# Optimization experiments

Measured on AMD Instinct MI355X. Metric: run time of the kernel, lower is better.

The kernel has to match this reference:

```python
import jax, jax.numpy as jnp
import numpy as np

B, C, H, W, P = 16, 512, 64, 64, 32


def setup_inputs() -> dict:
    key = jax.random.key(0)
    k1, k2, k3 = jax.random.split(key, 3)
    inputs = jax.random.normal(k1, (B, C, H, W), dtype=jnp.float32)
    weight = jax.random.uniform(k2, (P, C, 1, 1), dtype=jnp.float32)
    smooth_factor = jax.random.normal(k3, (P,), dtype=jnp.float32)
    return {"inputs": inputs, "weight": weight, "smooth_factor": smooth_factor}


def reference(inputs, weight, smooth_factor):
    b, c, h, w = inputs.shape
    p = weight.shape[0]
    n = h * w
    centers = weight.reshape(p, c)                      # [P,C]
    x = inputs.reshape(b, c, n)                         # [B,C,N]

    # distance-based logits: 2<c,x> - |x|^2 - |c|^2, clamped at 0
    cx = jnp.einsum('pc,bcn->bpn', centers, x)          # [B,P,N]
    x_sq = jnp.sum(x * x, axis=1, keepdims=True)        # [B,1,N]
    c_sq = jnp.sum(centers * centers, axis=1)[None, :, None]  # [1,P,1]
    beta = jax.nn.sigmoid(smooth_factor)                # [P]
    logits = jnp.minimum(2.0 * cx - x_sq - c_sq, 0.0) / beta[None, :, None]
    assign = jax.nn.softmax(logits, axis=1)             # [B,P,N]

    # assignment-weighted pooling
    qx = jnp.einsum('bpn,bcn->bpc', assign, x)          # [B,P,C]
    sum_ass = jnp.clip(jnp.sum(assign, axis=2, keepdims=True), 1e-5)  # [B,P,1]
    sigma = jnp.sqrt(beta / 2.0)                        # [P]
    out = (qx / sum_ass - centers[None, :, :]) / sigma[None, :, None]

    # L2-normalize over channel dim (torch F.normalize, eps=1e-12)
    norm = jnp.sqrt(jnp.sum(out * out, axis=2, keepdims=True))
    outputs = out / jnp.maximum(norm, 1e-12)
    outputs_t = jnp.transpose(outputs, (0, 2, 1))       # [B,C,P]
    assign_map = assign.reshape(b, p, h, w)             # [B,P,H,W]
    return outputs_t, assign_map
```

## Files before the change

kernel.cpp:

```cpp
#include <hip/hip_runtime.h>

constexpr int BB = 16;
constexpr int CC = 512;
constexpr int PP = 32;
constexpr int NN = 4096;
constexpr int TN = 128;

using f32x4 = __attribute__((ext_vector_type(4))) float;
using bf16x8 = __attribute__((ext_vector_type(8))) short;
typedef unsigned int uint;

__device__ __forceinline__ ushort f2bf(float f) {
  unsigned u = __builtin_bit_cast(unsigned, f);
  u += 0x7FFFu + ((u >> 16) & 1u);
  return (ushort)(u >> 16);
}

__device__ __forceinline__ uint packbf(float f) {
  uint u = __builtin_bit_cast(uint, f);
  uint hi = (u + (0x7FFFu + ((u >> 16) & 1u))) >> 16;
  float hif = __builtin_bit_cast(float, hi << 16);
  float lof = f - hif;
  uint ul = __builtin_bit_cast(uint, lof);
  uint lo = (ul + (0x7FFFu + ((ul >> 16) & 1u))) >> 16;
  return (lo << 16) | hi;
}

struct BfPair { bf16x8 hi, lo; };

__device__ __forceinline__ BfPair unpack8(const uint* __restrict__ row, int co) {
  uint4 a = *(const uint4*)(row + co);
  uint4 b = *(const uint4*)(row + co + 4);
  union { bf16x8 v; uint d[4]; } H, L;
  H.d[0] = (a.x & 0xffffu) | (a.y << 16); L.d[0] = (a.x >> 16) | (a.y & 0xffff0000u);
  H.d[1] = (a.z & 0xffffu) | (a.w << 16); L.d[1] = (a.z >> 16) | (a.w & 0xffff0000u);
  H.d[2] = (b.x & 0xffffu) | (b.y << 16); L.d[2] = (b.x >> 16) | (b.y & 0xffff0000u);
  H.d[3] = (b.z & 0xffffu) | (b.w << 16); L.d[3] = (b.z >> 16) | (b.w & 0xffff0000u);
  return {H.v, L.v};
}

__global__ __launch_bounds__(64) void prep_kernel(
    const float* __restrict__ w, const float* __restrict__ sf,
    float* __restrict__ beta, float* __restrict__ rbeta,
    float* __restrict__ csq, float* __restrict__ sum_ass) {
  int p = blockIdx.x;
  int t = threadIdx.x;
  if (t < 16) sum_ass[p * 16 + t] = 0.f;
  float s = 0.f;
  for (int i = t; i < CC; i += 64) {
    float v = w[p * CC + i];
    s = fmaf(v, v, s);
  }
#pragma unroll
  for (int off = 32; off; off >>= 1) s += __shfl_down(s, off);
  if (t == 0) {
    csq[p] = s;
    float e = __expf(-sf[p]);
    rbeta[p] = 1.f + e;
    beta[p] = 1.f / (1.f + e);
  }
}

__global__ __launch_bounds__(256, 3) void assign_kernel(
    const float* __restrict__ x, const float* __restrict__ w,
    const float* __restrict__ rbeta, const float* __restrict__ csq,
    float* __restrict__ assign_out, float* __restrict__ sum_ass) {
  __shared__ uint xpk[128][68];
  __shared__ uint cpk[32][68];
  __shared__ float xsqw[4][4][32];
  __shared__ float xsqf[128];

  int tid = threadIdx.x;
  int wv = tid >> 6, lane = tid & 63;
  int l15 = lane & 15, lg = lane >> 4;
  int b = blockIdx.x >> 5;
  int n0 = (blockIdx.x & 31) * TN;

  int c_s = tid >> 2;
  int q = tid & 3;
  int p_s = tid >> 3;
  int cq8 = (tid & 7) << 3;

  const float* xb = x + (size_t)b * CC * NN + n0 + q * 32;
  const float* wb = w + (size_t)p_s * CC + cq8;

  f32x4 acc[2][2];
#pragma unroll
  for (int i = 0; i < 2; ++i)
#pragma unroll
    for (int j = 0; j < 2; ++j) acc[i][j] = {0.f, 0.f, 0.f, 0.f};
  float sq[32];
#pragma unroll
  for (int i = 0; i < 32; ++i) sq[i] = 0.f;

  float4 xr[8], wr0, wr1;
#pragma unroll
  for (int i = 0; i < 8; ++i)
    xr[i] = *(const float4*)&xb[(size_t)c_s * NN + i * 4];
  wr0 = *(const float4*)&wb[0];
  wr1 = *(const float4*)&wb[4];
#pragma unroll
  for (int i = 0; i < 8; ++i) {
    float4 v = xr[i];
    sq[4 * i + 0] = fmaf(v.x, v.x, sq[4 * i + 0]);
    sq[4 * i + 1] = fmaf(v.y, v.y, sq[4 * i + 1]);
    sq[4 * i + 2] = fmaf(v.z, v.z, sq[4 * i + 2]);
    sq[4 * i + 3] = fmaf(v.w, v.w, sq[4 * i + 3]);
    int nr = q * 32 + i * 4;
    xpk[nr + 0][c_s] = packbf(v.x);
    xpk[nr + 1][c_s] = packbf(v.y);
    xpk[nr + 2][c_s] = packbf(v.z);
    xpk[nr + 3][c_s] = packbf(v.w);
  }
  {
    uint4 u0 = {packbf(wr0.x), packbf(wr0.y), packbf(wr0.z), packbf(wr0.w)};
    uint4 u1 = {packbf(wr1.x), packbf(wr1.y), packbf(wr1.z), packbf(wr1.w)};
    *(uint4*)&cpk[p_s][cq8] = u0;
    *(uint4*)&cpk[p_s][cq8 + 4] = u1;
  }
  __syncthreads();

  for (int c0 = 0; c0 < CC; c0 += 64) {
    bool more = (c0 + 64 < CC);
    if (more) {
#pragma unroll
      for (int i = 0; i < 8; ++i)
        xr[i] = *(const float4*)&xb[(size_t)(c0 + 64 + c_s) * NN + i * 4];
      wr0 = *(const float4*)&wb[c0 + 64];
      wr1 = *(const float4*)&wb[c0 + 64 + 4];
    }
#pragma unroll
    for (int ks = 0; ks < 2; ++ks) {
      int co = ks * 32 + lg * 8;
      BfPair A0 = unpack8(&cpk[l15][0], co);
      BfPair A1 = unpack8(&cpk[l15 + 16][0], co);
      BfPair B0 = unpack8(&xpk[wv * 32 + l15][0], co);
      BfPair B1 = unpack8(&xpk[wv * 32 + 16 + l15][0], co);
      acc[0][0] = __builtin_amdgcn_mfma_f32_16x16x32_bf16(A0.hi, B0.hi, acc[0][0], 0, 0, 0);
      acc[0][1] = __builtin_amdgcn_mfma_f32_16x16x32_bf16(A0.hi, B1.hi, acc[0][1], 0, 0, 0);
      acc[1][0] = __builtin_amdgcn_mfma_f32_16x16x32_bf16(A1.hi, B0.hi, acc[1][0], 0, 0, 0);
      acc[1][1] = __builtin_amdgcn_mfma_f32_16x16x32_bf16(A1.hi, B1.hi, acc[1][1], 0, 0, 0);
      acc[0][0] = __builtin_amdgcn_mfma_f32_16x16x32_bf16(A0.hi, B0.lo, acc[0][0], 0, 0, 0);
      acc[0][1] = __builtin_amdgcn_mfma_f32_16x16x32_bf16(A0.hi, B1.lo, acc[0][1], 0, 0, 0);
      acc[1][0] = __builtin_amdgcn_mfma_f32_16x16x32_bf16(A1.hi, B0.lo, acc[1][0], 0, 0, 0);
      acc[1][1] = __builtin_amdgcn_mfma_f32_16x16x32_bf16(A1.hi, B1.lo, acc[1][1], 0, 0, 0);
      acc[0][0] = __builtin_amdgcn_mfma_f32_16x16x32_bf16(A0.lo, B0.hi, acc[0][0], 0, 0, 0);
      acc[0][1] = __builtin_amdgcn_mfma_f32_16x16x32_bf16(A0.lo, B1.hi, acc[0][1], 0, 0, 0);
      acc[1][0] = __builtin_amdgcn_mfma_f32_16x16x32_bf16(A1.lo, B0.hi, acc[1][0], 0, 0, 0);
      acc[1][1] = __builtin_amdgcn_mfma_f32_16x16x32_bf16(A1.lo, B1.hi, acc[1][1], 0, 0, 0);
    }
    if (more) {
      __syncthreads();
#pragma unroll
      for (int i = 0; i < 8; ++i) {
        float4 v = xr[i];
        sq[4 * i + 0] = fmaf(v.x, v.x, sq[4 * i + 0]);
        sq[4 * i + 1] = fmaf(v.y, v.y, sq[4 * i + 1]);
        sq[4 * i + 2] = fmaf(v.z, v.z, sq[4 * i + 2]);
        sq[4 * i + 3] = fmaf(v.w, v.w, sq[4 * i + 3]);
        int nr = q * 32 + i * 4;
        xpk[nr + 0][c_s] = packbf(v.x);
        xpk[nr + 1][c_s] = packbf(v.y);
        xpk[nr + 2][c_s] = packbf(v.z);
        xpk[nr + 3][c_s] = packbf(v.w);
      }
      uint4 u0 = {packbf(wr0.x), packbf(wr0.y), packbf(wr0.z), packbf(wr0.w)};
      uint4 u1 = {packbf(wr1.x), packbf(wr1.y), packbf(wr1.z), packbf(wr1.w)};
      *(uint4*)&cpk[p_s][cq8] = u0;
      *(uint4*)&cpk[p_s][cq8 + 4] = u1;
      __syncthreads();
    }
  }

#pragma unroll
  for (int i = 0; i < 32; ++i) {
    sq[i] += __shfl_xor(sq[i], 4);
    sq[i] += __shfl_xor(sq[i], 8);
    sq[i] += __shfl_xor(sq[i], 16);
    sq[i] += __shfl_xor(sq[i], 32);
  }
  if ((lane >> 2) == 0) {
#pragma unroll
    for (int i = 0; i < 32; ++i) xsqw[wv][lane & 3][i] = sq[i];
  }
  __syncthreads();
  if (tid < 128)
    xsqf[tid] = xsqw[0][tid >> 5][tid & 31] + xsqw[1][tid >> 5][tid & 31] +
                xsqw[2][tid >> 5][tid & 31] + xsqw[3][tid >> 5][tid & 31];
  __syncthreads();

  float xsqn0 = xsqf[wv * 32 + l15];
  float xsqn1 = xsqf[wv * 32 + 16 + l15];

  float csqv[2][4], rbv[2][4];
#pragma unroll
  for (int pf = 0; pf < 2; ++pf)
#pragma unroll
    for (int i = 0; i < 4; ++i) {
      int p = pf * 16 + lg * 4 + i;
      csqv[pf][i] = csq[p];
      rbv[pf][i] = rbeta[p];
    }

  float L[2][2][4];
  float m0 = -3.4e38f, m1 = -3.4e38f;
#pragma unroll
  for (int pf = 0; pf < 2; ++pf)
#pragma unroll
    for (int i = 0; i < 4; ++i) {
      float l0 = fminf(2.f * acc[pf][0][i] - xsqn0 - csqv[pf][i], 0.f) * rbv[pf][i];
      float l1 = fminf(2.f * acc[pf][1][i] - xsqn1 - csqv[pf][i], 0.f) * rbv[pf][i];
      L[pf][0][i] = l0; L[pf][1][i] = l1;
      m0 = fmaxf(m0, l0); m1 = fmaxf(m1, l1);
    }
  m0 = fmaxf(m0, __shfl_xor(m0, 16)); m0 = fmaxf(m0, __shfl_xor(m0, 32));
  m1 = fmaxf(m1, __shfl_xor(m1, 16)); m1 = fmaxf(m1, __shfl_xor(m1, 32));
  float s0 = 0.f, s1 = 0.f;
#pragma unroll
  for (int pf = 0; pf < 2; ++pf)
#pragma unroll
    for (int i = 0; i < 4; ++i) {
      float e0 = __expf(L[pf][0][i] - m0);
      float e1 = __expf(L[pf][1][i] - m1);
      L[pf][0][i] = e0; L[pf][1][i] = e1;
      s0 += e0; s1 += e1;
    }
  s0 += __shfl_xor(s0, 16); s0 += __shfl_xor(s0, 32);
  s1 += __shfl_xor(s1, 16); s1 += __shfl_xor(s1, 32);
  float inv0 = 1.f / s0, inv1 = 1.f / s1;

  float* aoB = assign_out + (size_t)b * PP * NN + n0 + wv * 32 + l15;
  float sa[2][4];
#pragma unroll
  for (int pf = 0; pf < 2; ++pf)
#pragma unroll
    for (int i = 0; i < 4; ++i) {
      int p = pf * 16 + lg * 4 + i;
      float a0 = L[pf][0][i] * inv0;
      float a1 = L[pf][1][i] * inv1;
      aoB[(size_t)p * NN] = a0;
      aoB[(size_t)p * NN + 16] = a1;
      sa[pf][i] = a0 + a1;
    }
#pragma unroll
  for (int pf = 0; pf < 2; ++pf)
#pragma unroll
    for (int i = 0; i < 4; ++i) {
      float v = sa[pf][i];
      v += __shfl_xor(v, 1); v += __shfl_xor(v, 2);
      v += __shfl_xor(v, 4); v += __shfl_xor(v, 8);
      if (l15 == 0) atomicAdd(&sum_ass[b * PP + pf * 16 + lg * 4 + i], v);
    }
}

__global__ __launch_bounds__(256) void qx_kernel(
    const float* __restrict__ x, const float* __restrict__ assign,
    float* __restrict__ qx_part) {
  __shared__ ushort xbf[128][136];
  __shared__ ushort abf[32][136];

  int tid = threadIdx.x;
  int b = blockIdx.y;
  int kc = blockIdx.x >> 2;
  int ct = blockIdx.x & 3;
  int wv = tid >> 6, lane = tid & 63;
  int l15 = lane & 15, lg = lane >> 4;

  const float* xb = x + ((size_t)b * CC + ct * 128) * NN + kc * 512;
  const float* ab = assign + (size_t)b * PP * NN + kc * 512;

  int c_s = tid >> 1;
  int nh  = (tid & 1) << 6;
  int p_s = tid >> 3;
  int na  = (tid & 7) << 4;

  f32x4 acc[2][2];
#pragma unroll
  for (int i = 0; i < 2; ++i)
#pragma unroll
    for (int j = 0; j < 2; ++j) acc[i][j] = {0.f, 0.f, 0.f, 0.f};

  for (int ch = 0; ch < 4; ++ch) {
    int nb = ch * 128;
    if (ch) __syncthreads();
#pragma unroll
    for (int h = 0; h < 2; ++h) {
      float4 v[8];
#pragma unroll
      for (int i = 0; i < 8; ++i)
        v[i] = *(const float4*)&xb[(size_t)c_s * NN + nb + nh + h * 32 + i * 4];
#pragma unroll
      for (int i = 0; i < 8; ++i) {
        ushort4 u;
        u.x = f2bf(v[i].x); u.y = f2bf(v[i].y);
        u.z = f2bf(v[i].z); u.w = f2bf(v[i].w);
        *(ushort4*)&xbf[c_s][nh + h * 32 + i * 4] = u;
      }
    }
    {
      float4 v[4];
#pragma unroll
      for (int i = 0; i < 4; ++i)
        v[i] = *(const float4*)&ab[(size_t)p_s * NN + nb + na + i * 4];
#pragma unroll
      for (int i = 0; i < 4; ++i) {
        ushort4 u;
        u.x = f2bf(v[i].x); u.y = f2bf(v[i].y);
        u.z = f2bf(v[i].z); u.w = f2bf(v[i].w);
        *(ushort4*)&abf[p_s][na + i * 4] = u;
      }
    }
    __syncthreads();
#pragma unroll
    for (int ks = 0; ks < 4; ++ks) {
      int nf = ks * 32 + lg * 8;
      bf16x8 a0 = *(const bf16x8*)&abf[l15][nf];
      bf16x8 a1 = *(const bf16x8*)&abf[16 + l15][nf];
      bf16x8 b0 = *(const bf16x8*)&xbf[wv * 32 + l15][nf];
      bf16x8 b1 = *(const bf16x8*)&xbf[wv * 32 + 16 + l15][nf];
      acc[0][0] = __builtin_amdgcn_mfma_f32_16x16x32_bf16(a0, b0, acc[0][0], 0, 0, 0);
      acc[0][1] = __builtin_amdgcn_mfma_f32_16x16x32_bf16(a0, b1, acc[0][1], 0, 0, 0);
      acc[1][0] = __builtin_amdgcn_mfma_f32_16x16x32_bf16(a1, b0, acc[1][0], 0, 0, 0);
      acc[1][1] = __builtin_amdgcn_mfma_f32_16x16x32_bf16(a1, b1, acc[1][1], 0, 0, 0);
    }
  }

#pragma unroll
  for (int pf = 0; pf < 2; ++pf)
#pragma unroll
    for (int cf = 0; cf < 2; ++cf)
#pragma unroll
      for (int i = 0; i < 4; ++i) {
        int p = pf * 16 + lg * 4 + i;
        int c = ct * 128 + wv * 32 + cf * 16 + l15;
        qx_part[(((size_t)kc * BB + b) * PP + p) * CC + c] = acc[pf][cf][i];
      }
}

__global__ __launch_bounds__(256) void finalize_kernel(
    const float* __restrict__ qx_part, const float* __restrict__ w,
    const float* __restrict__ beta, const float* __restrict__ sum_ass,
    float* __restrict__ out_t) {
  int b = blockIdx.x >> 5;
  int p = blockIdx.x & 31;
  int tid = threadIdx.x;
  int wave = tid >> 6, lane = tid & 63;

  float inv_sa = 1.f / fmaxf(sum_ass[b * PP + p], 1e-5f);
  float rsig = rsqrtf(0.5f * beta[p]);

  int c0 = tid, c1 = tid + 256;
  float q0 = 0.f, q1 = 0.f;
#pragma unroll
  for (int kc = 0; kc < 8; ++kc) {
    const float* row = qx_part + (((size_t)kc * BB + b) * PP + p) * CC;
    q0 += row[c0];
    q1 += row[c1];
  }
  const float* wrow = w + (size_t)p * CC;
  float t0 = (q0 * inv_sa - wrow[c0]) * rsig;
  float t1 = (q1 * inv_sa - wrow[c1]) * rsig;

  float nr = t0 * t0 + t1 * t1;
#pragma unroll
  for (int off = 32; off; off >>= 1) nr += __shfl_down(nr, off);
  __shared__ float red[4];
  if (lane == 0) red[wave] = nr;
  __syncthreads();
  float norm2 = red[0] + red[1] + red[2] + red[3];
  float scale = 1.f / fmaxf(sqrtf(norm2), 1e-12f);

  float* ob = out_t + (size_t)b * CC * PP + p;
  ob[(size_t)c0 * PP] = t0 * scale;
  ob[(size_t)c1 * PP] = t1 * scale;
}

extern "C" void kernel_launch(void* const* d_in, const int* in_sizes, int n_in,
                              void* d_out, int out_size, void* d_ws,
                              size_t ws_size, hipStream_t stream) {
  const float* x = (const float*)d_in[0];
  const float* w = (const float*)d_in[1];
  const float* sf = (const float*)d_in[2];

  float* out_t = (float*)d_out;
  float* assign = out_t + (size_t)BB * CC * PP;

  float* ws = (float*)d_ws;
  float* beta = ws;
  float* rbeta = ws + 32;
  float* csq = ws + 64;
  float* sum_ass = ws + 96;
  float* qx_part = ws + 608;

  prep_kernel<<<PP, 64, 0, stream>>>(w, sf, beta, rbeta, csq, sum_ass);
  assign_kernel<<<BB * 32, 256, 0, stream>>>(x, w, rbeta, csq, assign,
                                             sum_ass);
  qx_kernel<<<dim3(32, BB), 256, 0, stream>>>(x, assign, qx_part);
  finalize_kernel<<<BB * PP, 256, 0, stream>>>(qx_part, w, beta, sum_ass,
                                               out_t);
}
```

Baseline: 88.89 us.

## Fuse assignment-weighted pooling into assign kernel with atomic qx accumulation

The qx GEMM moves into the assign kernel. Softmax outputs go straight to shared memory as bf16, and the block re-reads its own x tile in 128-channel chunks to run the MFMA pooling. Partial qx results are accumulated with global atomicAdd into a memset-zeroed buffer, which removes the separate qx kernel, its re-read of the assignment map, and the partial-sum reduction in finalize. In exchange there are many float atomics (512 blocks each adding 32x512 values), a second pass over x that may hit in cache, and a summation order that is no longer deterministic.

Result: slower. 95.37 us (+7.3%).

```diff
diff --git a/kernel.cpp b/kernel.cpp
--- a/kernel.cpp
+++ b/kernel.cpp
@@ -42,10 +42,9 @@
 __global__ __launch_bounds__(64) void prep_kernel(
     const float* __restrict__ w, const float* __restrict__ sf,
     float* __restrict__ beta, float* __restrict__ rbeta,
-    float* __restrict__ csq, float* __restrict__ sum_ass) {
+    float* __restrict__ csq) {
   int p = blockIdx.x;
   int t = threadIdx.x;
-  if (t < 16) sum_ass[p * 16 + t] = 0.f;
   float s = 0.f;
   for (int i = t; i < CC; i += 64) {
     float v = w[p * CC + i];
@@ -61,14 +60,17 @@
   }
 }
 
-__global__ __launch_bounds__(256, 3) void assign_kernel(
+__global__ __launch_bounds__(256, 3) void fused_kernel(
     const float* __restrict__ x, const float* __restrict__ w,
-    const float* __restrict__ rbeta, const float* __restrict__ csq,
-    float* __restrict__ assign_out, float* __restrict__ sum_ass) {
+    const float* __restrict__ rbeta_, const float* __restrict__ csq_,
+    float* __restrict__ assign_out, float* __restrict__ sum_ass,
+    float* __restrict__ qx) {
   __shared__ uint xpk[128][68];
   __shared__ uint cpk[32][68];
   __shared__ float xsqw[4][4][32];
   __shared__ float xsqf[128];
+  ushort(*xt)[136] = (ushort(*)[136]) & xpk[0][0];
+  ushort(*abf)[136] = (ushort(*)[136]) & cpk[0][0];
 
   int tid = threadIdx.x;
   int wv = tid >> 6, lane = tid & 63;
@@ -198,8 +200,8 @@
 #pragma unroll
     for (int i = 0; i < 4; ++i) {
       int p = pf * 16 + lg * 4 + i;
-      csqv[pf][i] = csq[p];
-      rbv[pf][i] = rbeta[p];
+      csqv[pf][i] = csq_[p];
+      rbv[pf][i] = rbeta_[p];
     }
 
   float L[2][2][4];
@@ -230,7 +232,6 @@
   float inv0 = 1.f / s0, inv1 = 1.f / s1;
 
   float* aoB = assign_out + (size_t)b * PP * NN + n0 + wv * 32 + l15;
-  float sa[2][4];
 #pragma unroll
   for (int pf = 0; pf < 2; ++pf)
 #pragma unroll
@@ -240,105 +241,68 @@
       float a1 = L[pf][1][i] * inv1;
       aoB[(size_t)p * NN] = a0;
       aoB[(size_t)p * NN + 16] = a1;
-      sa[pf][i] = a0 + a1;
-    }
-#pragma unroll
-  for (int pf = 0; pf < 2; ++pf)
-#pragma unroll
-    for (int i = 0; i < 4; ++i) {
-      float v = sa[pf][i];
+      abf[p][wv * 32 + l15] = f2bf(a0);
+      abf[p][wv * 32 + 16 + l15] = f2bf(a1);
+      float v = a0 + a1;
       v += __shfl_xor(v, 1); v += __shfl_xor(v, 2);
       v += __shfl_xor(v, 4); v += __shfl_xor(v, 8);
-      if (l15 == 0) atomicAdd(&sum_ass[b * PP + pf * 16 + lg * 4 + i], v);
-    }
-}
-
-__global__ __launch_bounds__(256) void qx_kernel(
-    const float* __restrict__ x, const float* __restrict__ assign,
-    float* __restrict__ qx_part) {
-  __shared__ ushort xbf[128][136];
-  __shared__ ushort abf[32][136];
-
-  int tid = threadIdx.x;
-  int b = blockIdx.y;
-  int kc = blockIdx.x >> 2;
-  int ct = blockIdx.x & 3;
-  int wv = tid >> 6, lane = tid & 63;
-  int l15 = lane & 15, lg = lane >> 4;
-
-  const float* xb = x + ((size_t)b * CC + ct * 128) * NN + kc * 512;
-  const float* ab = assign + (size_t)b * PP * NN + kc * 512;
-
-  int c_s = tid >> 1;
-  int nh  = (tid & 1) << 6;
-  int p_s = tid >> 3;
-  int na  = (tid & 7) << 4;
-
-  f32x4 acc[2][2];
-#pragma unroll
-  for (int i = 0; i < 2; ++i)
-#pragma unroll
-    for (int j = 0; j < 2; ++j) acc[i][j] = {0.f, 0.f, 0.f, 0.f};
+      if (l15 == 0) atomicAdd(&sum_ass[b * PP + p], v);
+    }
+
+  int c_s2 = tid >> 1;
+  int nh2 = (tid & 1) << 6;
+  const float* xg = x + (size_t)b * CC * NN + n0;
 
   for (int ch = 0; ch < 4; ++ch) {
-    int nb = ch * 128;
-    if (ch) __syncthreads();
+    __syncthreads();
 #pragma unroll
     for (int h = 0; h < 2; ++h) {
       float4 v[8];
 #pragma unroll
       for (int i = 0; i < 8; ++i)
-        v[i] = *(const float4*)&xb[(size_t)c_s * NN + nb + nh + h * 32 + i * 4];
+        v[i] = *(const float4*)&xg[(size_t)(ch * 128 + c_s2) * NN + nh2 + h * 32 + i * 4];
 #pragma unroll
       for (int i = 0; i < 8; ++i) {
         ushort4 u;
         u.x = f2bf(v[i].x); u.y = f2bf(v[i].y);
         u.z = f2bf(v[i].z); u.w = f2bf(v[i].w);
-        *(ushort4*)&xbf[c_s][nh + h * 32 + i * 4] = u;
+        *(ushort4*)&xt[c_s2][nh2 + h * 32 + i * 4] = u;
       }
     }
-    {
-      float4 v[4];
-#pragma unroll
-      for (int i = 0; i < 4; ++i)
-        v[i] = *(const float4*)&ab[(size_t)p_s * NN + nb + na + i * 4];
-#pragma unroll
-      for (int i = 0; i < 4; ++i) {
-        ushort4 u;
-        u.x = f2bf(v[i].x); u.y = f2bf(v[i].y);
-        u.z = f2bf(v[i].z); u.w = f2bf(v[i].w);
-        *(ushort4*)&abf[p_s][na + i * 4] = u;
+    __syncthreads();
+
+    f32x4 q2[2][2];
+#pragma unroll
+    for (int pf = 0; pf < 2; ++pf)
+#pragma unroll
+      for (int cf = 0; cf < 2; ++cf) q2[pf][cf] = {0.f, 0.f, 0.f, 0.f};
+#pragma unroll
+    for (int ks = 0; ks < 4; ++ks) {
+      int ko = ks * 32 + lg * 8;
+      bf16x8 A0 = *(const bf16x8*)&abf[l15][ko];
+      bf16x8 A1 = *(const bf16x8*)&abf[l15 + 16][ko];
+#pragma unroll
+      for (int cf = 0; cf < 2; ++cf) {
+        bf16x8 Bv = *(const bf16x8*)&xt[wv * 32 + cf * 16 + l15][ko];
+        q2[0][cf] = __builtin_amdgcn_mfma_f32_16x16x32_bf16(A0, Bv, q2[0][cf], 0, 0, 0);
+        q2[1][cf] = __builtin_amdgcn_mfma_f32_16x16x32_bf16(A1, Bv, q2[1][cf], 0, 0, 0);
       }
     }
-    __syncthreads();
-#pragma unroll
-    for (int ks = 0; ks < 4; ++ks) {
-      int nf = ks * 32 + lg * 8;
-      bf16x8 a0 = *(const bf16x8*)&abf[l15][nf];
-      bf16x8 a1 = *(const bf16x8*)&abf[16 + l15][nf];
-      bf16x8 b0 = *(const bf16x8*)&xbf[wv * 32 + l15][nf];
-      bf16x8 b1 = *(const bf16x8*)&xbf[wv * 32 + 16 + l15][nf];
-      acc[0][0] = __builtin_amdgcn_mfma_f32_16x16x32_bf16(a0, b0, acc[0][0], 0, 0, 0);
-      acc[0][1] = __builtin_amdgcn_mfma_f32_16x16x32_bf16(a0, b1, acc[0][1], 0, 0, 0);
-      acc[1][0] = __builtin_amdgcn_mfma_f32_16x16x32_bf16(a1, b0, acc[1][0], 0, 0, 0);
-      acc[1][1] = __builtin_amdgcn_mfma_f32_16x16x32_bf16(a1, b1, acc[1][1], 0, 0, 0);
-    }
-  }
-
-#pragma unroll
-  for (int pf = 0; pf < 2; ++pf)
-#pragma unroll
-    for (int cf = 0; cf < 2; ++cf)
-#pragma unroll
-      for (int i = 0; i < 4; ++i) {
-        int p = pf * 16 + lg * 4 + i;
-        int c = ct * 128 + wv * 32 + cf * 16 + l15;
-        qx_part[(((size_t)kc * BB + b) * PP + p) * CC + c] = acc[pf][cf][i];
-      }
+#pragma unroll
+    for (int pf = 0; pf < 2; ++pf)
+#pragma unroll
+      for (int cf = 0; cf < 2; ++cf)
+#pragma unroll
+        for (int i = 0; i < 4; ++i) {
+          int p = pf * 16 + lg * 4 + i;
+          int c = ch * 128 + wv * 32 + cf * 16 + l15;
+          atomicAdd(&qx[((size_t)b * PP + p) * CC + c], q2[pf][cf][i]);
+        }
+  }
 }
 
 __global__ __launch_bounds__(256) void finalize_kernel(
-    const float* __restrict__ qx_part, const float* __restrict__ w,
+    const float* __restrict__ qx, const float* __restrict__ w,
     const float* __restrict__ beta, const float* __restrict__ sum_ass,
     float* __restrict__ out_t) {
   int b = blockIdx.x >> 5;
@@ -350,16 +314,10 @@
   float rsig = rsqrtf(0.5f * beta[p]);
 
   int c0 = tid, c1 = tid + 256;
-  float q0 = 0.f, q1 = 0.f;
-#pragma unroll
-  for (int kc = 0; kc < 8; ++kc) {
-    const float* row = qx_part + (((size_t)kc * BB + b) * PP + p) * CC;
-    q0 += row[c0];
-    q1 += row[c1];
-  }
+  const float* qrow = qx + ((size_t)b * PP + p) * CC;
   const float* wrow = w + (size_t)p * CC;
-  float t0 = (q0 * inv_sa - wrow[c0]) * rsig;
-  float t1 = (q1 * inv_sa - wrow[c1]) * rsig;
+  float t0 = (qrow[c0] * inv_sa - wrow[c0]) * rsig;
+  float t1 = (qrow[c1] * inv_sa - wrow[c1]) * rsig;
 
   float nr = t0 * t0 + t1 * t1;
 #pragma unroll
@@ -390,12 +348,12 @@
   float* rbeta = ws + 32;
   float* csq = ws + 64;
   float* sum_ass = ws + 96;
-  float* qx_part = ws + 608;
-
-  prep_kernel<<<PP, 64, 0, stream>>>(w, sf, beta, rbeta, csq, sum_ass);
-  assign_kernel<<<BB * 32, 256, 0, stream>>>(x, w, rbeta, csq, assign,
-                                             sum_ass);
-  qx_kernel<<<dim3(32, BB), 256, 0, stream>>>(x, assign, qx_part);
-  finalize_kernel<<<BB * PP, 256, 0, stream>>>(qx_part, w, beta, sum_ass,
-                                               out_t);
-}
+  float* qx = ws + 608;
+
+  hipMemsetAsync(sum_ass, 0, (512 + (size_t)BB * PP * CC) * sizeof(float),
+                 stream);
+  prep_kernel<<<PP, 64, 0, stream>>>(w, sf, beta, rbeta, csq);
+  fused_kernel<<<BB * 32, 256, 0, stream>>>(x, w, rbeta, csq, assign,
+                                            sum_ass, qx);
+  finalize_kernel<<<BB * PP, 256, 0, stream>>>(qx, w, beta, sum_ass, out_t);
+}
```
